# Kernel tuning notes

Hardware: AMD Instinct MI355X
Metric: run time of the kernel (lower is better)

The kernel has to match this reference:

```python
import jax, jax.numpy as jnp
import numpy as np

D_MODEL = 2048
N_HEADS = 16
D_K = D_MODEL // N_HEADS


def setup_inputs() -> dict:
    key = jax.random.key(0)
    k1, k2, k3 = jax.random.split(key, 3)
    x = jax.random.normal(k1, (2, 2048, D_MODEL), dtype=jnp.float32)
    # torch Linear convention: weight [out_features, in_features], y = x @ W.T
    W_qkv = jax.random.normal(k2, (3 * D_MODEL, D_MODEL), dtype=jnp.float32) * (D_MODEL ** -0.5)
    W_out = jax.random.normal(k3, (D_MODEL, D_MODEL), dtype=jnp.float32) * (D_MODEL ** -0.5)
    return {"x": x, "W_qkv": W_qkv, "W_out": W_out}


def reference(x, W_qkv, W_out):
    batch, seq_len, d_model = x.shape
    qkv = jnp.einsum('bsd,ed->bse', x, W_qkv)  # [B,S,3*D]
    qkv = qkv.reshape(batch, seq_len, 3, N_HEADS, D_K)
    qkv = jnp.transpose(qkv, (2, 0, 3, 1, 4))  # [3,B,H,S,Dk]
    Q, K, V = qkv[0], qkv[1], qkv[2]
    scores = jnp.einsum('bhqd,bhkd->bhqk', Q, K) / jnp.sqrt(jnp.float32(D_K))
    causal_mask = jnp.triu(jnp.ones((seq_len, seq_len), dtype=bool), k=1)
    scores = jnp.where(causal_mask, jnp.float32(-jnp.inf), scores)
    attn = jax.nn.softmax(scores, axis=-1)
    out = jnp.einsum('bhqk,bhkd->bhqd', attn, V)  # [B,H,S,Dk]
    out = jnp.transpose(out, (0, 2, 1, 3)).reshape(batch, seq_len, d_model)
    return jnp.einsum('bsd,ed->bse', out, W_out)
```

## Files before the change

kernel.cpp:

```cpp
#include <hip/hip_runtime.h>
#include <hip/hip_bf16.h>


typedef short bf16x8 __attribute__((ext_vector_type(8)));
typedef float f32x4  __attribute__((ext_vector_type(4)));

#define MFMA(a, b, c) __builtin_amdgcn_mfma_f32_16x16x32_bf16((a), (b), (c), 0, 0, 0)

#define GLDS16(gp, lp) __builtin_amdgcn_global_load_lds(                        \
    (const __attribute__((address_space(1))) void*)(gp),                        \
    (__attribute__((address_space(3))) void*)(lp), 16, 0, 0)

static __device__ __forceinline__ unsigned short f2bf(float f) {
    __hip_bfloat16 h = __float2bfloat16(f);
    return *reinterpret_cast<unsigned short*>(&h);
}

__global__ __launch_bounds__(256) void cvt3_f32_bf16(const float* __restrict__ x,
                                                     const float* __restrict__ wq,
                                                     const float* __restrict__ wo,
                                                     unsigned short* __restrict__ xb,
                                                     unsigned short* __restrict__ wqb,
                                                     unsigned short* __restrict__ wob) {
    const int i = blockIdx.x * 256 + threadIdx.x;
    const float* src; unsigned short* dst; int k;
    if (i < 2097152)      { src = x;  dst = xb;  k = i; }
    else if (i < 5242880) { src = wq; dst = wqb; k = i - 2097152; }
    else                  { src = wo; dst = wob; k = i - 5242880; }
    float4 v = reinterpret_cast<const float4*>(src)[k];
    ushort4 o;
    o.x = f2bf(v.x); o.y = f2bf(v.y); o.z = f2bf(v.z); o.w = f2bf(v.w);
    reinterpret_cast<ushort4*>(dst)[k] = o;
}

template <bool BF16OUT>
__global__ __launch_bounds__(256) void gemm_bt(const unsigned short* __restrict__ A,
                                               const unsigned short* __restrict__ W,
                                               void* __restrict__ Cout,
                                               int M, int N, int K) {
    __shared__ unsigned short As[128 * 32];
    __shared__ unsigned short Bs[128 * 32];
    const int tid = threadIdx.x;
    const int w = tid >> 6, lane = tid & 63;
    const int fr = lane & 15, fq = lane >> 4;
    const int m0 = blockIdx.y * 128, n0 = blockIdx.x * 128;
    const int wr = w >> 1, wc = w & 1;

    f32x4 acc[4][4];
#pragma unroll
    for (int a = 0; a < 4; a++)
#pragma unroll
        for (int b = 0; b < 4; b++) acc[a][b] = f32x4{0.f, 0.f, 0.f, 0.f};

    const int srow = w * 16 + (lane >> 2);
    const int scol = (lane & 3) * 8;

    for (int kt = 0; kt < K; kt += 32) {
        __syncthreads();
#pragma unroll
        for (int it = 0; it < 2; ++it) {
            const unsigned short* ga = A + (size_t)(m0 + it * 64 + srow) * K + kt + scol;
            unsigned short* la = As + (it * 64 + w * 16) * 32;
            GLDS16(ga, la);
            const unsigned short* gb = W + (size_t)(n0 + it * 64 + srow) * K + kt + scol;
            unsigned short* lb = Bs + (it * 64 + w * 16) * 32;
            GLDS16(gb, lb);
        }
        asm volatile("s_waitcnt vmcnt(0)" ::: "memory");
        __syncthreads();

        bf16x8 af[4], bfr[4];
#pragma unroll
        for (int mi = 0; mi < 4; mi++)
            af[mi] = *reinterpret_cast<const bf16x8*>(As + (wr * 64 + mi * 16 + fr) * 32 + fq * 8);
#pragma unroll
        for (int ni = 0; ni < 4; ni++)
            bfr[ni] = *reinterpret_cast<const bf16x8*>(Bs + (wc * 64 + ni * 16 + fr) * 32 + fq * 8);
#pragma unroll
        for (int mi = 0; mi < 4; mi++)
#pragma unroll
            for (int ni = 0; ni < 4; ni++)
                acc[mi][ni] = MFMA(af[mi], bfr[ni], acc[mi][ni]);
    }

#pragma unroll
    for (int mi = 0; mi < 4; mi++) {
#pragma unroll
        for (int i = 0; i < 4; i++) {
            const int row = m0 + wr * 64 + mi * 16 + fq * 4 + i;
            const size_t base = (size_t)row * N + n0 + wc * 64 + fr;
#pragma unroll
            for (int ni = 0; ni < 4; ni++) {
                if (BF16OUT)
                    ((unsigned short*)Cout)[base + ni * 16] = f2bf(acc[mi][ni][i]);
                else
                    ((float*)Cout)[base + ni * 16] = acc[mi][ni][i];
            }
        }
    }
}

__global__ __launch_bounds__(256) void transpose_v(const unsigned short* __restrict__ qkv,
                                                   unsigned short* __restrict__ vT) {
    __shared__ unsigned short t[32][33];
    const int b = blockIdx.z, ts = blockIdx.x, tu = blockIdx.y;
    const int i = threadIdx.x >> 5, j = threadIdx.x & 31;
#pragma unroll
    for (int ii = 0; ii < 4; ++ii) {
        const int row = i + ii * 8;
        t[row][j] = qkv[(size_t)(b * 2048 + ts * 32 + row) * 6144 + 4096 + tu * 32 + j];
    }
    __syncthreads();
#pragma unroll
    for (int ii = 0; ii < 4; ++ii) {
        const int row = i + ii * 8;
        vT[(size_t)(b * 2048 + tu * 32 + row) * 2048 + ts * 32 + j] = t[j][row];
    }
}

#define SC2 (0.08838834764831845f * 1.4426950408889634f)
#define MREF 20.0f

__global__ __launch_bounds__(256, 2) void attn_fwd(const unsigned short* __restrict__ qkv,
                                                   const unsigned short* __restrict__ vT,
                                                   unsigned short* __restrict__ ao) {
    __shared__ __align__(16) char Kt[2][16384];
    __shared__ __align__(16) char Vt[2][16384];
    __shared__ __align__(16) unsigned short Ps[4][16 * 72];
    const int tid = threadIdx.x;
    const int w = tid >> 6, lane = tid & 63;
    const int fr = lane & 15, fq = lane >> 4;
    const int t = blockIdx.x;
    const int bh = t & 31;
    const int j = t >> 5;
    const int b = bh >> 4, h = bh & 15;

    const unsigned short* Qb = qkv + (size_t)b * 2048 * 6144 + h * 128;
    const unsigned short* Kb = qkv + (size_t)b * 2048 * 6144 + (16 + h) * 128;
    const unsigned short* Vb = vT + (size_t)bh * 128 * 2048;

    unsigned short* Pw = &Ps[w][0];
    const bf16x8 onesf = {0x3F80, 0x3F80, 0x3F80, 0x3F80, 0x3F80, 0x3F80, 0x3F80, 0x3F80};

    auto stage = [&](int kbs, int bufi) {
        const int k0s = kbs * 64;
        if (w < 2) {
#pragma unroll
            for (int q = 0; q < 8; ++q) {
                const int i = w * 8 + q;
                const int r = 4 * i + (lane >> 4);
                const int ce = ((((lane & 15) * 16) ^ ((r & 7) << 4))) >> 1;
                GLDS16(Kb + (size_t)(k0s + r) * 6144 + ce, &Kt[bufi][i * 1024]);
            }
        } else {
#pragma unroll
            for (int q = 0; q < 8; ++q) {
                const int i = (w - 2) * 8 + q;
                const int r = 8 * i + (lane >> 3);
                const int ce = ((lane & 7) ^ ((lane >> 3) & 7)) * 8;
                GLDS16(Vb + (size_t)r * 2048 + k0s + ce, &Vt[bufi][i * 1024]);
            }
        }
    };

#pragma unroll 1
    for (int seg = 0; seg < 2; ++seg) {
        const int g = seg ? j : 31 - j;
        const int q0 = g * 64 + w * 16;
        const int nb = g + 1;

        bf16x8 qf[4];
        {
            const unsigned short* qr = Qb + (size_t)(q0 + fr) * 6144 + fq * 8;
#pragma unroll
            for (int c = 0; c < 4; c++) qf[c] = *reinterpret_cast<const bf16x8*>(qr + c * 32);
        }

        f32x4 acc[8];
#pragma unroll
        for (int f = 0; f < 8; f++) acc[f] = f32x4{0.f, 0.f, 0.f, 0.f};
        f32x4 accL = f32x4{0.f, 0.f, 0.f, 0.f};

        int cur = 0;
        stage(0, 0);
        __syncthreads();

        for (int kb = 0; kb < nb; ++kb) {
            if (kb + 1 < nb) stage(kb + 1, cur ^ 1);
            const int k0 = kb * 64;
            const char* Kl = &Kt[cur][0];
            const char* Vl = &Vt[cur][0];

            f32x4 s[4];
#pragma unroll
            for (int th = 0; th < 2; ++th) {
                bf16x8 kf[2][4];
#pragma unroll
                for (int t2 = 0; t2 < 2; ++t2) {
                    const int tt = th * 2 + t2;
#pragma unroll
                    for (int c = 0; c < 4; ++c)
                        kf[t2][c] = *reinterpret_cast<const bf16x8*>(
                            Kl + (tt * 16 + fr) * 256 + ((c * 64 + fq * 16) ^ ((fr & 7) << 4)));
                }
                f32x4 a0 = f32x4{0.f, 0.f, 0.f, 0.f}, a1 = f32x4{0.f, 0.f, 0.f, 0.f};
                __builtin_amdgcn_s_setprio(1);
#pragma unroll
                for (int c = 0; c < 4; ++c) {
                    a0 = MFMA(qf[c], kf[0][c], a0);
                    a1 = MFMA(qf[c], kf[1][c], a1);
                }
                __builtin_amdgcn_s_setprio(0);
                s[th * 2] = a0; s[th * 2 + 1] = a1;
            }

            const bool diag = (kb == nb - 1);
#pragma unroll
            for (int i = 0; i < 4; ++i) {
                const int qrow = q0 + fq * 4 + i;
#pragma unroll
                for (int tt = 0; tt < 4; ++tt) {
                    float a = __builtin_fmaf(s[tt][i], SC2, -MREF);
                    if (diag && (k0 + tt * 16 + fr > qrow)) a = -__builtin_inff();
                    Pw[(fq * 4 + i) * 72 + tt * 16 + fr] = f2bf(exp2f(a));
                }
            }

#pragma unroll
            for (int h2 = 0; h2 < 2; ++h2) {
                bf16x8 pa = *reinterpret_cast<const bf16x8*>(Pw + fr * 72 + h2 * 32 + fq * 8);
                bf16x8 vf[8];
#pragma unroll
                for (int f = 0; f < 8; ++f)
                    vf[f] = *reinterpret_cast<const bf16x8*>(
                        Vl + (f * 16 + fr) * 128 + ((h2 * 64 + fq * 16) ^ ((fr & 7) << 4)));
                __builtin_amdgcn_s_setprio(1);
#pragma unroll
                for (int f = 0; f < 8; ++f) acc[f] = MFMA(pa, vf[f], acc[f]);
                accL = MFMA(pa, onesf, accL);
                __builtin_amdgcn_s_setprio(0);
            }

            __syncthreads();
            cur ^= 1;
        }

        float inv[4];
#pragma unroll
        for (int i = 0; i < 4; ++i) inv[i] = 1.0f / accL[i];
#pragma unroll
        for (int f = 0; f < 8; f++) {
#pragma unroll
            for (int i = 0; i < 4; i++) {
                const int qrow = q0 + fq * 4 + i;
                const float o = acc[f][i] * inv[i];
                ao[(size_t)(b * 2048 + qrow) * 2048 + h * 128 + f * 16 + fr] = f2bf(o);
            }
        }
    }
}

extern "C" void kernel_launch(void* const* d_in, const int* in_sizes, int n_in,
                              void* d_out, int out_size, void* d_ws, size_t ws_size,
                              hipStream_t stream) {
    const float* x    = (const float*)d_in[0];
    const float* Wqkv = (const float*)d_in[1];
    const float* Wout = (const float*)d_in[2];
    float* out = (float*)d_out;

    char* ws = (char*)d_ws;
    unsigned short* xb    = (unsigned short*)(ws);
    unsigned short* wqkvb = (unsigned short*)(ws + (size_t)(16 << 20));
    unsigned short* woutb = (unsigned short*)(ws + (size_t)(40 << 20));
    unsigned short* qkvb  = (unsigned short*)(ws + (size_t)(48 << 20));
    unsigned short* vTb   = (unsigned short*)(ws + (size_t)(16 << 20));
    unsigned short* attnb = (unsigned short*)(ws);

    cvt3_f32_bf16<<<24576, 256, 0, stream>>>(x, Wqkv, Wout, xb, wqkvb, woutb);

    gemm_bt<true><<<dim3(48, 32), 256, 0, stream>>>(xb, wqkvb, qkvb, 4096, 6144, 2048);

    transpose_v<<<dim3(64, 64, 2), 256, 0, stream>>>(qkvb, vTb);

    attn_fwd<<<512, 256, 0, stream>>>(qkvb, vTb, attnb);

    gemm_bt<false><<<dim3(16, 32), 256, 0, stream>>>(attnb, woutb, out, 4096, 2048, 2048);
}
```

Before: 284.4 us.

## Use XCD-aware persistent tile mapping for QKV projection GEMM

Replaces the 2D grid launch of the QKV GEMM with a dedicated kernel using 768 blocks, each computing two adjacent 128x128 output tiles. Block IDs are remapped so that blocks landing on the same XCD share a group of M rows, which is meant to improve L2 reuse of A and W tiles. The cost is fewer blocks (768 instead of 1536), so less latency hiding across blocks and possible tail imbalance.

```diff
diff --git a/kernel.cpp b/kernel.cpp
--- a/kernel.cpp
+++ b/kernel.cpp
@@ -33,6 +33,77 @@
     reinterpret_cast<ushort4*>(dst)[k] = o;
 }
 
+__global__ __launch_bounds__(256) void gemm_qkv(const unsigned short* __restrict__ A,
+                                                const unsigned short* __restrict__ W,
+                                                unsigned short* __restrict__ Cout) {
+    constexpr int M = 4096, N = 6144, K = 2048;
+    __shared__ unsigned short As[128 * 32];
+    __shared__ unsigned short Bs[128 * 32];
+    const int tid = threadIdx.x;
+    const int w = tid >> 6, lane = tid & 63;
+    const int fr = lane & 15, fq = lane >> 4;
+    const int wr = w >> 1, wc = w & 1;
+    const int srow = w * 16 + (lane >> 2);
+    const int scol = (lane & 3) * 8;
+
+    const int bid = blockIdx.x;
+    const int xcd = bid & 7, r = bid >> 3;
+    const int mi = xcd * 4 + (r & 3);
+    const int chunk = r >> 2;
+
+#pragma unroll 1
+    for (int t = 0; t < 2; ++t) {
+        const int ni = chunk * 2 + t;
+        const int m0 = mi * 128, n0 = ni * 128;
+
+        f32x4 acc[4][4];
+#pragma unroll
+        for (int a = 0; a < 4; a++)
+#pragma unroll
+            for (int b = 0; b < 4; b++) acc[a][b] = f32x4{0.f, 0.f, 0.f, 0.f};
+
+        for (int kt = 0; kt < K; kt += 32) {
+            __syncthreads();
+#pragma unroll
+            for (int it = 0; it < 2; ++it) {
+                const unsigned short* ga = A + (size_t)(m0 + it * 64 + srow) * K + kt + scol;
+                unsigned short* la = As + (it * 64 + w * 16) * 32;
+                GLDS16(ga, la);
+                const unsigned short* gb = W + (size_t)(n0 + it * 64 + srow) * K + kt + scol;
+                unsigned short* lb = Bs + (it * 64 + w * 16) * 32;
+                GLDS16(gb, lb);
+            }
+            asm volatile("s_waitcnt vmcnt(0)" ::: "memory");
+            __syncthreads();
+
+            bf16x8 af[4], bfr[4];
+#pragma unroll
+            for (int mj = 0; mj < 4; mj++)
+                af[mj] = *reinterpret_cast<const bf16x8*>(As + (wr * 64 + mj * 16 + fr) * 32 + fq * 8);
+#pragma unroll
+            for (int nj = 0; nj < 4; nj++)
+                bfr[nj] = *reinterpret_cast<const bf16x8*>(Bs + (wc * 64 + nj * 16 + fr) * 32 + fq * 8);
+#pragma unroll
+            for (int mj = 0; mj < 4; mj++)
+#pragma unroll
+                for (int nj = 0; nj < 4; nj++)
+                    acc[mj][nj] = MFMA(af[mj], bfr[nj], acc[mj][nj]);
+        }
+
+#pragma unroll
+        for (int mj = 0; mj < 4; mj++) {
+#pragma unroll
+            for (int i = 0; i < 4; i++) {
+                const int row = m0 + wr * 64 + mj * 16 + fq * 4 + i;
+                const size_t base = (size_t)row * N + n0 + wc * 64 + fr;
+#pragma unroll
+                for (int nj = 0; nj < 4; nj++)
+                    Cout[base + nj * 16] = f2bf(acc[mj][nj][i]);
+            }
+        }
+    }
+}
+
 template <bool BF16OUT>
 __global__ __launch_bounds__(256) void gemm_bt(const unsigned short* __restrict__ A,
                                                const unsigned short* __restrict__ W,
@@ -278,7 +349,7 @@
 
     cvt3_f32_bf16<<<24576, 256, 0, stream>>>(x, Wqkv, Wout, xb, wqkvb, woutb);
 
-    gemm_bt<true><<<dim3(48, 32), 256, 0, stream>>>(xb, wqkvb, qkvb, 4096, 6144, 2048);
+    gemm_qkv<<<768, 256, 0, stream>>>(xb, wqkvb, qkvb);
 
     transpose_v<<<dim3(64, 64, 2), 256, 0, stream>>>(qkvb, vTb);
 
```

After: 330.9 us. 1.16x slower.

## Deepen GEMM K-tile to 64 with XOR-swizzled LDS layout and MFMA priority

Applied to the files above, without the earlier changes.

Both projection GEMMs now stage a 64-wide K slice per iteration instead of 32, which halves the number of barrier/wait rounds per tile. The LDS layout is XOR-swizzled on 16-byte chunks so the fragment reads avoid bank conflicts. s_setprio raises wave priority around the MFMA bursts. The costs are double the LDS footprint per block, which may lower occupancy, and more index arithmetic for the swizzle.

```diff
diff --git a/kernel.cpp b/kernel.cpp
--- a/kernel.cpp
+++ b/kernel.cpp
@@ -34,12 +34,12 @@
 }
 
 template <bool BF16OUT>
-__global__ __launch_bounds__(256) void gemm_bt(const unsigned short* __restrict__ A,
-                                               const unsigned short* __restrict__ W,
-                                               void* __restrict__ Cout,
-                                               int M, int N, int K) {
-    __shared__ unsigned short As[128 * 32];
-    __shared__ unsigned short Bs[128 * 32];
+__global__ __launch_bounds__(256) void gemm_bt64(const unsigned short* __restrict__ A,
+                                                 const unsigned short* __restrict__ W,
+                                                 void* __restrict__ Cout,
+                                                 int M, int N, int K) {
+    __shared__ unsigned short As[128 * 64];
+    __shared__ unsigned short Bs[128 * 64];
     const int tid = threadIdx.x;
     const int w = tid >> 6, lane = tid & 63;
     const int fr = lane & 15, fq = lane >> 4;
@@ -52,35 +52,44 @@
 #pragma unroll
         for (int b = 0; b < 4; b++) acc[a][b] = f32x4{0.f, 0.f, 0.f, 0.f};
 
-    const int srow = w * 16 + (lane >> 2);
-    const int scol = (lane & 3) * 8;
-
-    for (int kt = 0; kt < K; kt += 32) {
+    const int srow = lane >> 3;
+    const int sce  = ((lane & 7) ^ (lane >> 3)) * 8;
+
+    for (int kt = 0; kt < K; kt += 64) {
         __syncthreads();
 #pragma unroll
-        for (int it = 0; it < 2; ++it) {
-            const unsigned short* ga = A + (size_t)(m0 + it * 64 + srow) * K + kt + scol;
-            unsigned short* la = As + (it * 64 + w * 16) * 32;
-            GLDS16(ga, la);
-            const unsigned short* gb = W + (size_t)(n0 + it * 64 + srow) * K + kt + scol;
-            unsigned short* lb = Bs + (it * 64 + w * 16) * 32;
-            GLDS16(gb, lb);
+        for (int q = 0; q < 4; ++q) {
+            const int i = w * 4 + q;
+            const int r = i * 8 + srow;
+            GLDS16(A + (size_t)(m0 + r) * K + kt + sce, As + i * 512);
+            GLDS16(W + (size_t)(n0 + r) * K + kt + sce, Bs + i * 512);
         }
         asm volatile("s_waitcnt vmcnt(0)" ::: "memory");
         __syncthreads();
 
-        bf16x8 af[4], bfr[4];
-#pragma unroll
-        for (int mi = 0; mi < 4; mi++)
-            af[mi] = *reinterpret_cast<const bf16x8*>(As + (wr * 64 + mi * 16 + fr) * 32 + fq * 8);
-#pragma unroll
-        for (int ni = 0; ni < 4; ni++)
-            bfr[ni] = *reinterpret_cast<const bf16x8*>(Bs + (wc * 64 + ni * 16 + fr) * 32 + fq * 8);
-#pragma unroll
-        for (int mi = 0; mi < 4; mi++)
-#pragma unroll
-            for (int ni = 0; ni < 4; ni++)
-                acc[mi][ni] = MFMA(af[mi], bfr[ni], acc[mi][ni]);
+#pragma unroll
+        for (int kk = 0; kk < 2; ++kk) {
+            bf16x8 af[4], bfr[4];
+#pragma unroll
+            for (int mi = 0; mi < 4; mi++) {
+                const int row = wr * 64 + mi * 16 + fr;
+                af[mi] = *reinterpret_cast<const bf16x8*>(
+                    As + row * 64 + ((((kk * 64 + fq * 16) ^ ((fr & 7) << 4))) >> 1));
+            }
+#pragma unroll
+            for (int ni = 0; ni < 4; ni++) {
+                const int row = wc * 64 + ni * 16 + fr;
+                bfr[ni] = *reinterpret_cast<const bf16x8*>(
+                    Bs + row * 64 + ((((kk * 64 + fq * 16) ^ ((fr & 7) << 4))) >> 1));
+            }
+            __builtin_amdgcn_s_setprio(1);
+#pragma unroll
+            for (int mi = 0; mi < 4; mi++)
+#pragma unroll
+                for (int ni = 0; ni < 4; ni++)
+                    acc[mi][ni] = MFMA(af[mi], bfr[ni], acc[mi][ni]);
+            __builtin_amdgcn_s_setprio(0);
+        }
     }
 
 #pragma unroll
@@ -278,11 +287,11 @@
 
     cvt3_f32_bf16<<<24576, 256, 0, stream>>>(x, Wqkv, Wout, xb, wqkvb, woutb);
 
-    gemm_bt<true><<<dim3(48, 32), 256, 0, stream>>>(xb, wqkvb, qkvb, 4096, 6144, 2048);
+    gemm_bt64<true><<<dim3(48, 32), 256, 0, stream>>>(xb, wqkvb, qkvb, 4096, 6144, 2048);
 
     transpose_v<<<dim3(64, 64, 2), 256, 0, stream>>>(qkvb, vTb);
 
     attn_fwd<<<512, 256, 0, stream>>>(qkvb, vTb, attnb);
 
-    gemm_bt<false><<<dim3(16, 32), 256, 0, stream>>>(attnb, woutb, out, 4096, 2048, 2048);
-}
+    gemm_bt64<false><<<dim3(16, 32), 256, 0, stream>>>(attnb, woutb, out, 4096, 2048, 2048);
+}
```

After: 245.1 us. 1.16x faster.
